# Kernel tuning notes

Hardware: AMD Instinct MI355X
Metric: run time of the kernel (lower is better)

## Reference

```python
import jax, jax.numpy as jnp
import numpy as np

B, T, E, H, D = 2, 2048, 1024, 16, 64   # batch, seq, n_embd, heads, head_dim
C, P, BF, MH, R, F4 = 64, 64, 256, 128, 8, 4096  # ctx_dim, prototypes, basis, mod hidden, gate rank, 4*n_embd


def _rms(x):
    return x * jax.lax.rsqrt(jnp.mean(x * x, axis=-1, keepdims=True) + 1e-6)


def _rotary(x, cos, sin):
    d = x.shape[-1] // 2
    x1, x2 = x[..., :d], x[..., d:]
    return jnp.concatenate([x1 * cos + x2 * sin, -x1 * sin + x2 * cos], axis=-1)


def _ln(x, g, b):
    mu = jnp.mean(x, axis=-1, keepdims=True)
    v = jnp.mean(jnp.square(x - mu), axis=-1, keepdims=True)
    return (x - mu) * jax.lax.rsqrt(v + 1e-5) * g + b


def _remixed(x, ctx, bw, lg, lb, tm, bias, m1w, m1b, m2w, m2b, ogw, ogb, ogB, ogs):
    # RemixedLinear: basis proj -> LayerNorm -> context sigmoid gate -> template mixing -> low-rank output gate
    h = _ln(x @ bw.T, lg, lb)                                              # [B,T,basis]
    gl = jax.nn.gelu(ctx @ m1w.T + m1b, approximate=False) @ m2w.T + m2b   # basis_modulator MLP
    gate_basis = jax.nn.sigmoid(gl)                                        # gate_temperature = 1.0, dense gate
    gate_out = 1.0 + jnp.tanh(ogs * ((ctx @ ogw.T + ogb) @ ogB))           # low-rank output gate
    return (h * gate_basis) @ tm.T * gate_out + bias


def _forward(x, cos, sin, wq, wk, wv, wo, cb_qw, protos,
             fc_bw, fc_lg, fc_lb, fc_tm, fc_b, fc_m1w, fc_m1b, fc_m2w, fc_m2b, fc_ogw, fc_ogb, fc_ogB, fc_ogs,
             pj_bw, pj_lg, pj_lb, pj_tm, pj_b, pj_m1w, pj_m1b, pj_m2w, pj_m2b, pj_ogw, pj_ogb, pj_ogB, pj_ogs):
    b, t, _ = x.shape
    # --- attention with rotary embeddings ---
    xn = _rms(x)
    q = _rotary((xn @ wq.T).reshape(b, t, H, D), cos, sin)
    k = _rotary((xn @ wk.T).reshape(b, t, H, D), cos, sin)
    v = (xn @ wv.T).reshape(b, t, H, D)
    s = jnp.einsum('bqhd,bkhd->bhqk', q, k) * (D ** -0.5)
    mask = jnp.tril(jnp.ones((t, t), dtype=bool))
    s = jnp.where(mask, s, jnp.finfo(s.dtype).min)
    a = jax.nn.softmax(s, axis=-1)
    attn_out = jnp.einsum('bhqk,bkhd->bqhd', a, v).reshape(b, t, E) @ wo.T
    x = x + attn_out
    # --- ContextBank: soft lookup into prototype vocabulary ---
    xn2 = _rms(x)
    cq = xn2 @ cb_qw.T                                  # [B,T,C]
    w = jax.nn.softmax((cq @ protos.T) * (C ** -0.5), axis=-1)
    ctx = w @ protos                                    # [B,T,C]
    # --- RemixedFeedForward: RemixedLinear -> relu^2 -> RemixedLinear ---
    h = _remixed(xn2, ctx, fc_bw, fc_lg, fc_lb, fc_tm, fc_b, fc_m1w, fc_m1b, fc_m2w, fc_m2b, fc_ogw, fc_ogb, fc_ogB, fc_ogs)
    h = jnp.square(jax.nn.relu(h))
    y = _remixed(h, ctx, pj_bw, pj_lg, pj_lb, pj_tm, pj_b, pj_m1w, pj_m1b, pj_m2w, pj_m2b, pj_ogw, pj_ogb, pj_ogB, pj_ogs)
    return x + y


def setup_inputs():
    key = jax.random.key(0)
    ks = jax.random.split(key, 24)
    g = lambda i, shape, s=0.02: jax.random.normal(ks[i], shape, jnp.float32) * s
    t = jnp.arange(T, dtype=jnp.float32)
    inv = 1.0 / (10000.0 ** (jnp.arange(0, D, 2, dtype=jnp.float32) / D))
    ang = t[:, None] * inv                              # [T, D/2]
    return dict(
        x=jax.random.normal(ks[0], (B, T, E), jnp.float32),
        cos=jnp.cos(ang)[None, :, None, :], sin=jnp.sin(ang)[None, :, None, :],
        wq=g(1, (E, E)), wk=g(2, (E, E)), wv=g(3, (E, E)), wo=g(4, (E, E)),
        cb_qw=g(5, (C, E)), protos=g(6, (P, C)),
        fc_bw=g(7, (BF, E)), fc_lg=jnp.ones((BF,)), fc_lb=jnp.zeros((BF,)),
        fc_tm=g(8, (F4, BF), 0.05), fc_b=jnp.zeros((F4,)),
        fc_m1w=g(9, (MH, C)), fc_m1b=jnp.zeros((MH,)),
        fc_m2w=g(10, (BF, MH)), fc_m2b=jnp.zeros((BF,)),
        fc_ogw=g(11, (R, C)), fc_ogb=jnp.zeros((R,)),
        fc_ogB=g(12, (R, F4)), fc_ogs=jnp.full((1,), 0.1, jnp.float32),
        pj_bw=g(13, (BF, F4)), pj_lg=jnp.ones((BF,)), pj_lb=jnp.zeros((BF,)),
        pj_tm=g(14, (E, BF), 0.05), pj_b=jnp.zeros((E,)),
        pj_m1w=g(15, (MH, C)), pj_m1b=jnp.zeros((MH,)),
        pj_m2w=g(16, (BF, MH)), pj_m2b=jnp.zeros((BF,)),
        pj_ogw=g(17, (R, C)), pj_ogb=jnp.zeros((R,)),
        pj_ogB=g(18, (R, E)), pj_ogs=jnp.full((1,), 0.1, jnp.float32),
    )


def reference(x, cos, sin, wq, wk, wv, wo, cb_qw, protos,
              fc_bw, fc_lg, fc_lb, fc_tm, fc_b, fc_m1w, fc_m1b, fc_m2w, fc_m2b, fc_ogw, fc_ogb, fc_ogB, fc_ogs,
              pj_bw, pj_lg, pj_lb, pj_tm, pj_b, pj_m1w, pj_m1b, pj_m2w, pj_m2b, pj_ogw, pj_ogb, pj_ogB, pj_ogs):
    return _forward(x, cos, sin, wq, wk, wv, wo, cb_qw, protos,
                    fc_bw, fc_lg, fc_lb, fc_tm, fc_b, fc_m1w, fc_m1b, fc_m2w, fc_m2b, fc_ogw, fc_ogb, fc_ogB, fc_ogs,
                    pj_bw, pj_lg, pj_lb, pj_tm, pj_b, pj_m1w, pj_m1b, pj_m2w, pj_m2b, pj_ogw, pj_ogb, pj_ogB, pj_ogs)
```

## Files before the change

### kernel.cpp

```cpp
#include <hip/hip_runtime.h>
#include <hip/hip_bf16.h>

typedef unsigned short u16;
typedef unsigned int u32;
typedef __attribute__((ext_vector_type(8))) short bf16x8;
typedef __attribute__((ext_vector_type(4))) float f32x4;
typedef __attribute__((ext_vector_type(4))) u16 u16x4;

#define DEVFN __device__ __forceinline__

DEVFN u16 f2b(float f) {
  u32 u = __builtin_bit_cast(u32, f);
  return (u16)((u + 0x7FFFu + ((u >> 16) & 1u)) >> 16);
}
DEVFN float b2f(u16 b) { return __builtin_bit_cast(float, (u32)b << 16); }
DEVFN u32 cvtpk(float lo, float hi) {
  u32 r;
  asm("v_cvt_pk_bf16_f32 %0, %1, %2" : "=v"(r) : "v"(lo), "v"(hi));
  return r;
}

DEVFN void gll16(const void* g, void* l) {
  __builtin_amdgcn_global_load_lds((const __attribute__((address_space(1))) void*)g,
                                   (__attribute__((address_space(3))) void*)l, 16, 0, 0);
}
#define BARRIER() __builtin_amdgcn_s_barrier()

template <int N> DEVFN void waitvm() {
  if constexpr (N == 0) asm volatile("s_waitcnt vmcnt(0)" ::: "memory");
  else if constexpr (N == 1) asm volatile("s_waitcnt vmcnt(1)" ::: "memory");
  else if constexpr (N == 2) asm volatile("s_waitcnt vmcnt(2)" ::: "memory");
  else if constexpr (N == 3) asm volatile("s_waitcnt vmcnt(3)" ::: "memory");
  else if constexpr (N == 4) asm volatile("s_waitcnt vmcnt(4)" ::: "memory");
  else if constexpr (N == 5) asm volatile("s_waitcnt vmcnt(5)" ::: "memory");
  else if constexpr (N == 6) asm volatile("s_waitcnt vmcnt(6)" ::: "memory");
  else asm volatile("s_waitcnt vmcnt(8)" ::: "memory");
}

constexpr int Tc = 2048, Ec = 1024, Hc = 16, Cc = 64, BFc = 256, F4c = 4096;
constexpr int Mc = 2 * Tc;
constexpr float C8 = 0.18033688f;
constexpr float NEG2LOG2E = -2.8853901f;

constexpr size_t MB = 1ull << 20;
constexpr size_t O_XN  = 0;
constexpr size_t O_HBF = 8 * MB;
constexpr size_t O_QB  = 40 * MB;
constexpr size_t O_H1  = 40 * MB;
constexpr size_t O_A2  = 45 * MB;
constexpr size_t O_KB  = 48 * MB;
constexpr size_t O_H2  = 48 * MB;
constexpr size_t O_VBF = 56 * MB;
constexpr size_t O_CQ  = 64 * MB;
constexpr size_t O_GO1 = 68 * MB + 512 * 1024;
constexpr size_t O_GO2 = 68 * MB + 640 * 1024;
constexpr size_t O_GB1 = 69 * MB;
constexpr size_t O_VT  = 72 * MB;
constexpr size_t O_GB2 = 73 * MB;
constexpr size_t O_A1  = 77 * MB;
constexpr size_t O_X2  = 80 * MB;
constexpr size_t O_WQ  = 96 * MB, O_WK = 98 * MB, O_WV = 100 * MB, O_WO = 102 * MB;
constexpr size_t O_CBQ = 104 * MB;
constexpr size_t O_FCBW = O_CBQ + 128 * 1024;
constexpr size_t O_FCTM = 105 * MB;
constexpr size_t O_PJBW = 107 * MB;
constexpr size_t O_PJTM = 109 * MB;

struct Cvt9 {
  const float* s[9];
  u16* d[9];
  int cum[10];
};
__global__ __launch_bounds__(256) void k_cvt(Cvt9 a) {
  int i = blockIdx.x * 256 + threadIdx.x;
  int seg = 0;
  #pragma unroll
  for (int s = 1; s < 9; s++) seg += (i >= a.cum[s]);
  int off = i - a.cum[seg];
  float4 v = *(const float4*)&a.s[seg][(size_t)off * 4];
  u16x4 o; o.x = f2b(v.x); o.y = f2b(v.y); o.z = f2b(v.z); o.w = f2b(v.w);
  *(u16x4*)&a.d[seg][(size_t)off * 4] = o;
}

DEVFN float bsum256(float v, float* sb) {
  #pragma unroll
  for (int off = 32; off; off >>= 1) v += __shfl_down(v, off);
  __syncthreads();
  if ((threadIdx.x & 63) == 0) sb[threadIdx.x >> 6] = v;
  __syncthreads();
  return (sb[0] + sb[1]) + (sb[2] + sb[3]);
}

__global__ __launch_bounds__(256) void k_rms(const float* __restrict__ x, u16* __restrict__ o) {
  __shared__ float sb[4];
  int row = blockIdx.x, tid = threadIdx.x;
  float4 v = *(const float4*)&x[(size_t)row * 1024 + tid * 4];
  float s = bsum256(v.x * v.x + v.y * v.y + v.z * v.z + v.w * v.w, sb);
  float r = rsqrtf(s * (1.f / 1024.f) + 1e-6f);
  u16x4 ov;
  ov.x = f2b(v.x * r); ov.y = f2b(v.y * r); ov.z = f2b(v.z * r); ov.w = f2b(v.w * r);
  *(u16x4*)&o[(size_t)row * 1024 + tid * 4] = ov;
}

__global__ __launch_bounds__(256) void k_vtrans(const u16* __restrict__ vb, u16* __restrict__ vt) {
  __shared__ u16 tl[64][65];
  int t0 = blockIdx.x * 64, bh = blockIdx.y;
  int b = bh >> 4, h = bh & 15, tid = threadIdx.x;
  #pragma unroll
  for (int rep = 0; rep < 16; rep++) {
    int idx = rep * 256 + tid, r = idx >> 6, c = idx & 63;
    tl[r][c] = vb[((size_t)(b * 2048 + t0 + r)) * 1024 + h * 64 + c];
  }
  __syncthreads();
  #pragma unroll
  for (int rep = 0; rep < 16; rep++) {
    int idx = rep * 256 + tid, d = idx >> 6, tt = idx & 63;
    vt[((size_t)bh * 64 + d) * 2048 + t0 + tt] = tl[tt][d];
  }
}

#define MFMA16(A, B, C) __builtin_amdgcn_mfma_f32_16x16x32_bf16(A, B, C, 0, 0, 0)
__global__ __launch_bounds__(256) void k_attn(const u16* __restrict__ Q, const u16* __restrict__ Kb,
                                              const u16* __restrict__ VT, u16* __restrict__ O) {
  const int i = blockIdx.x;
  const int wrk = (i & 7) * 64 + (i >> 3);
  const int hb = wrk >> 4, xp = wrk & 15;
  const int b = hb >> 4, h = hb & 15;
  const int tid = threadIdx.x, lane = tid & 63, w = tid >> 6;
  const int lr = lane & 15, lg = lane >> 4;
  const size_t TE = 2048ull * 1024ull;
  const u16* Qp = Q + (size_t)b * TE + (size_t)h * 64;
  const u16* Kp = Kb + (size_t)b * TE + (size_t)h * 64;
  const u16* Vp = VT + ((size_t)(b * 16 + h)) * 64ull * 2048ull;
  u16* Op = O + (size_t)b * TE + (size_t)h * 64;
  __shared__ __align__(16) u16 Ks[2][4096];
  __shared__ __align__(16) u16 Vs[2][4096];
  __shared__ __align__(16) u16 Ps[4][1024];
  auto stageKV = [&](int j0, int buf) {
    #pragma unroll
    for (int c = 0; c < 2; c++) {
      int u = c * 256 + tid;
      int row = u >> 3, slot = u & 7;
      int cg = slot ^ (row & 7);
      gll16(&Kp[(size_t)(j0 + row) * 1024 + cg * 8], &Ks[buf][u * 8]);
    }
    #pragma unroll
    for (int c = 0; c < 2; c++) {
      int u = c * 256 + tid;
      int row = u >> 3, slot = u & 7;
      int cg = slot ^ (row & 7);
      gll16(&Vp[(size_t)row * 2048 + j0 + cg * 8], &Vs[buf][u * 8]);
    }
  };
  auto run_tile = [&](int qb) {
    const int q0 = qb * 64, qw0 = q0 + w * 16;
    bf16x8 qf0 = *(const bf16x8*)&Qp[(size_t)(qw0 + lr) * 1024 + lg * 8];
    bf16x8 qf1 = *(const bf16x8*)&Qp[(size_t)(qw0 + lr) * 1024 + 32 + lg * 8];
    f32x4 o0 = {}, o1 = {}, o2 = {}, o3 = {};
    float m = -1e30f, l = 0.f;
    const int NT = qb + 1;
    stageKV(0, 0);
    int cur = 0;
    for (int it = 0; it < NT; it++) {
      if (it + 1 < NT) {
        stageKV((it + 1) * 64, cur ^ 1);
        waitvm<4>();
      } else {
        waitvm<0>();
      }
      BARRIER();
      const int j0 = it * 64;
      const u16* Kl = Ks[cur];
      const u16* Vl = Vs[cur];
      f32x4 c4[4];
      __builtin_amdgcn_s_setprio(1);
      #pragma unroll
      for (int kg = 0; kg < 4; kg++) {
        f32x4 cc = {};
        int r = kg * 16 + lr;
        bf16x8 ka0 = *(const bf16x8*)&Kl[r * 64 + ((lg ^ (lr & 7)) * 8)];
        bf16x8 ka1 = *(const bf16x8*)&Kl[r * 64 + (((4 + lg) ^ (lr & 7)) * 8)];
        cc = MFMA16(ka0, qf0, cc);
        cc = MFMA16(ka1, qf1, cc);
        c4[kg] = cc;
      }
      __builtin_amdgcn_s_setprio(0);
      float xs[16];
      #pragma unroll
      for (int kg = 0; kg < 4; kg++)
        #pragma unroll
        for (int r = 0; r < 4; r++) xs[kg * 4 + r] = c4[kg][r];
      if (it == NT - 1) {
        int q = qw0 + lr;
        #pragma unroll
        for (int kg = 0; kg < 4; kg++)
          #pragma unroll
          for (int r = 0; r < 4; r++)
            if (j0 + kg * 16 + lg * 4 + r > q) xs[kg * 4 + r] = -1e30f;
      }
      float tm = fmaxf(xs[0], xs[1]);
      tm = fmaxf(fmaxf(tm, xs[2]), xs[3]);
      tm = fmaxf(fmaxf(tm, xs[4]), xs[5]);
      tm = fmaxf(fmaxf(tm, xs[6]), xs[7]);
      tm = fmaxf(fmaxf(tm, xs[8]), xs[9]);
      tm = fmaxf(fmaxf(tm, xs[10]), xs[11]);
      tm = fmaxf(fmaxf(tm, xs[12]), xs[13]);
      tm = fmaxf(fmaxf(tm, xs[14]), xs[15]);
      tm = fmaxf(tm, __shfl_xor(tm, 16));
      tm = fmaxf(tm, __shfl_xor(tm, 32));
      if (!__all(tm <= m + 64.f)) {
        float mn = fmaxf(m, tm);
        float al = exp2f((m - mn) * C8);
        m = mn;
        l *= al;
        float ar0 = __shfl(al, lg * 4 + 0), ar1 = __shfl(al, lg * 4 + 1);
        float ar2 = __shfl(al, lg * 4 + 2), ar3 = __shfl(al, lg * 4 + 3);
        o0[0] *= ar0; o0[1] *= ar1; o0[2] *= ar2; o0[3] *= ar3;
        o1[0] *= ar0; o1[1] *= ar1; o1[2] *= ar2; o1[3] *= ar3;
        o2[0] *= ar0; o2[1] *= ar1; o2[2] *= ar2; o2[3] *= ar3;
        o3[0] *= ar0; o3[1] *= ar1; o3[2] *= ar2; o3[3] *= ar3;
      }
      const float mnC = -m * C8;
      float p[16], rs = 0.f;
      #pragma unroll
      for (int r = 0; r < 16; r++) { p[r] = exp2f(fmaf(xs[r], C8, mnC)); rs += p[r]; }
      rs += __shfl_xor(rs, 16);
      rs += __shfl_xor(rs, 32);
      l += rs;
      #pragma unroll
      for (int kg = 0; kg < 4; kg++) {
        int unit = (kg >> 1) * 64 + ((kg & 1) * 2 + (lg >> 1)) * 16 + lr;
        uint2 pk;
        pk.x = cvtpk(p[kg * 4 + 0], p[kg * 4 + 1]);
        pk.y = cvtpk(p[kg * 4 + 2], p[kg * 4 + 3]);
        *(uint2*)&Ps[w][unit * 8 + (lg & 1) * 4] = pk;
      }
      bf16x8 pa0 = *(const bf16x8*)&Ps[w][(lg * 16 + lr) * 8];
      bf16x8 pa1 = *(const bf16x8*)&Ps[w][(64 + lg * 16 + lr) * 8];
      __builtin_amdgcn_s_setprio(1);
      #pragma unroll
      for (int dg = 0; dg < 4; dg++) {
        int dr = dg * 16 + lr;
        bf16x8 v0 = *(const bf16x8*)&Vl[dr * 64 + ((lg ^ (lr & 7)) * 8)];
        bf16x8 v1 = *(const bf16x8*)&Vl[dr * 64 + (((4 + lg) ^ (lr & 7)) * 8)];
        f32x4& od = (dg == 0) ? o0 : (dg == 1) ? o1 : (dg == 2) ? o2 : o3;
        od = MFMA16(pa0, v0, od);
        od = MFMA16(pa1, v1, od);
      }
      __builtin_amdgcn_s_setprio(0);
      BARRIER();
      cur ^= 1;
    }
    float li0 = 1.f / __shfl(l, lg * 4 + 0), li1 = 1.f / __shfl(l, lg * 4 + 1);
    float li2 = 1.f / __shfl(l, lg * 4 + 2), li3 = 1.f / __shfl(l, lg * 4 + 3);
    #pragma unroll
    for (int r = 0; r < 4; r++) {
      float lir = (r == 0) ? li0 : (r == 1) ? li1 : (r == 2) ? li2 : li3;
      size_t ro = (size_t)(qw0 + lg * 4 + r) * 1024;
      Op[ro + lr]      = f2b(o0[r] * lir);
      Op[ro + 16 + lr] = f2b(o1[r] * lir);
      Op[ro + 32 + lr] = f2b(o2[r] * lir);
      Op[ro + 48 + lr] = f2b(o3[r] * lir);
    }
  };
  run_tile(xp);
  run_tile(31 - xp);
}

template <int BM, int BN, int WR, int WC, int EPI>
__global__ __launch_bounds__(256) void gemm_bt(
    const u16* __restrict__ A, const u16* __restrict__ Bw,
    float* __restrict__ Co, u16* __restrict__ Cb, u16* __restrict__ Cb2, u16* __restrict__ Cb3,
    int gM, int N, int K, int KS,
    const float* __restrict__ e0, const float* __restrict__ e1,
    const float* __restrict__ e2, const float* __restrict__ e3,
    const float* __restrict__ e4) {
  constexpr int WM = BM / WR, WN = BN / WC;
  constexpr int FM = WM / 16, FN = WN / 16;
  constexpr int ACH = BM / 64, BCH = BN / 64;
  static_assert(WR * WC == 4 && BM % 64 == 0 && BN % 64 == 0, "cfg");
  __shared__ __align__(16) u16 As[2][BM * 32];
  __shared__ __align__(16) u16 Bs[2][BN * 32];
  const int tid = threadIdx.x;
  const int lane = tid & 63, wid = tid >> 6;
  const int wr = wid / WC, wc = wid % WC;
  const int bm = blockIdx.y * BM, bn = blockIdx.x * BN;
  const int lr = lane & 15, lg = lane >> 4;
  const int arow0 = bm + wr * WM, bcol0 = bn + wc * WN;
  const int kbeg = blockIdx.z * KS, kend = kbeg + KS;
  f32x4 acc[FM][FN] = {};
  auto stage = [&](int k0, int buf) {
    #pragma unroll
    for (int c = 0; c < ACH; c++) {
      int u = c * 256 + tid;
      int row = u >> 2, slot = u & 3;
      int cg = slot ^ (row & 3) ^ ((row >> 2) & 3);
      gll16(&A[(size_t)(bm + row) * K + k0 + cg * 8], &As[buf][u * 8]);
    }
    #pragma unroll
    for (int c = 0; c < BCH; c++) {
      int u = c * 256 + tid;
      int row = u >> 2, slot = u & 3;
      int cg = slot ^ (row & 3) ^ ((row >> 2) & 3);
      gll16(&Bw[(size_t)(bn + row) * K + k0 + cg * 8], &Bs[buf][u * 8]);
    }
  };
  stage(kbeg, 0);
  int cur = 0;
  for (int k0 = kbeg; k0 < kend; k0 += 32) {
    if (k0 + 32 < kend) {
      stage(k0 + 32, cur ^ 1);
      waitvm<ACH + BCH>();
    } else {
      waitvm<0>();
    }
    BARRIER();
    const u16* Ab = As[cur];
    const u16* Bb = Bs[cur];
    bf16x8 af[FM], bfr[FN];
    #pragma unroll
    for (int i = 0; i < FM; i++) {
      int tr = wr * WM + i * 16 + lr;
      af[i] = *(const bf16x8*)&Ab[tr * 32 + ((lg ^ (tr & 3) ^ ((tr >> 2) & 3)) * 8)];
    }
    #pragma unroll
    for (int j = 0; j < FN; j++) {
      int tr = wc * WN + j * 16 + lr;
      bfr[j] = *(const bf16x8*)&Bb[tr * 32 + ((lg ^ (tr & 3) ^ ((tr >> 2) & 3)) * 8)];
    }
    #pragma unroll
    for (int i = 0; i < FM; i++)
      #pragma unroll
      for (int j = 0; j < FN; j++)
        acc[i][j] = __builtin_amdgcn_mfma_f32_16x16x32_bf16(af[i], bfr[j], acc[i][j], 0, 0, 0);
    BARRIER();
    cur ^= 1;
  }
  const int nb0 = bcol0 + lr;
  if constexpr (EPI == 0 || EPI == 2) {
    float* Cz = Co + (size_t)blockIdx.z * ((size_t)gM * N);
    #pragma unroll
    for (int i = 0; i < FM; i++)
      #pragma unroll
      for (int r = 0; r < 4; r++) {
        size_t mrow = (size_t)(arow0 + i * 16 + lg * 4 + r);
        #pragma unroll
        for (int j = 0; j < FN; j++) {
          float v = acc[i][j][r];
          if constexpr (EPI == 2) v += e4[mrow * N + nb0 + j * 16];
          Cz[mrow * N + nb0 + j * 16] = v;
        }
      }
  } else if constexpr (EPI == 9) {
    if (bn == 0) {
      #pragma unroll
      for (int i = 0; i < FM; i++)
        #pragma unroll
        for (int r = 0; r < 4; r++) {
          size_t mrow = (size_t)(arow0 + i * 16 + lg * 4 + r);
          #pragma unroll
          for (int j = 0; j < FN; j++)
            Co[mrow * 64 + nb0 + j * 16] = acc[i][j][r];
        }
    } else {
      float* H = (float*)Cb;
      const int c0 = bcol0 - 64 + lr;
      #pragma unroll
      for (int i = 0; i < FM; i++)
        #pragma unroll
        for (int r = 0; r < 4; r++) {
          size_t mrow = (size_t)(arow0 + i * 16 + lg * 4 + r);
          #pragma unroll
          for (int j = 0; j < FN; j++)
            H[mrow * 256 + c0 + j * 16] = acc[i][j][r];
        }
    }
  } else if constexpr (EPI == 8) {
    if (bn < 2048) {
      u16* dst = (bn < 1024) ? Cb : Cb2;
      const int nq0 = (bcol0 & 1023) + lr;
      #pragma unroll
      for (int i = 0; i < FM; i++)
        #pragma unroll
        for (int r = 0; r < 4; r++) {
          size_t mrow = (size_t)(arow0 + i * 16 + lg * 4 + r);
          int t = (int)(mrow & 2047);
          #pragma unroll
          for (int j = 0; j < 2; j++) {
            int d = lr + j * 16;
            float cth = e0[t * 32 + d], sth = e1[t * 32 + d];
            float x1 = acc[i][j][r], x2 = acc[i][j + 2][r];
            dst[mrow * 1024 + nq0 + j * 16]       = f2b(x1 * cth + x2 * sth);
            dst[mrow * 1024 + nq0 + (j + 2) * 16] = f2b(x2 * cth - x1 * sth);
          }
        }
    } else {
      const int nv0 = (bcol0 - 2048) + lr;
      #pragma unroll
      for (int i = 0; i < FM; i++)
        #pragma unroll
        for (int r = 0; r < 4; r++) {
          size_t mrow = (size_t)(arow0 + i * 16 + lg * 4 + r);
          #pragma unroll
          for (int j = 0; j < FN; j++)
            Cb3[mrow * 1024 + nv0 + j * 16] = f2b(acc[i][j][r]);
        }
    }
  } else {
    const float cg = e3[0] * NEG2LOG2E;
    float gB[FN][8], bias[FN];
    #pragma unroll
    for (int j = 0; j < FN; j++) {
      int n = nb0 + j * 16;
      bias[j] = e2[n];
      #pragma unroll
      for (int rr = 0; rr < 8; rr++) gB[j][rr] = e1[(size_t)rr * N + n];
    }
    #pragma unroll
    for (int i = 0; i < FM; i++)
      #pragma unroll
      for (int r = 0; r < 4; r++) {
        size_t mrow = (size_t)(arow0 + i * 16 + lg * 4 + r);
        float go8[8];
        #pragma unroll
        for (int rr = 0; rr < 8; rr++) go8[rr] = e0[mrow * 8 + rr];
        #pragma unroll
        for (int j = 0; j < FN; j++) {
          float d = 0.f;
          #pragma unroll
          for (int rr = 0; rr < 8; rr++) d += go8[rr] * gB[j][rr];
          float gate = 2.f * __builtin_amdgcn_rcpf(1.f + exp2f(cg * d));
          float v = acc[i][j][r] * gate + bias[j];
          if constexpr (EPI == 3) {
            v = fmaxf(v, 0.f); v *= v;
            Cb[mrow * N + nb0 + j * 16] = f2b(v);
          } else {
            v += e4[mrow * N + nb0 + j * 16];
            Co[mrow * N + nb0 + j * 16] = v;
          }
        }
      }
  }
}

__global__ __launch_bounds__(256) void k_ctxgate(
    const float* __restrict__ cq, const float* __restrict__ pr,
    const float* __restrict__ f_m1w, const float* __restrict__ f_m1b,
    const float* __restrict__ f_m2w, const float* __restrict__ f_m2b,
    const float* __restrict__ f_ogw, const float* __restrict__ f_ogb,
    const float* __restrict__ p_m1w, const float* __restrict__ p_m1b,
    const float* __restrict__ p_m2w, const float* __restrict__ p_m2b,
    const float* __restrict__ p_ogw, const float* __restrict__ p_ogb,
    float* __restrict__ gb1, float* __restrict__ go1,
    float* __restrict__ gb2, float* __restrict__ go2) {
  __shared__ float pl[64 * 65];
  __shared__ __align__(16) float cqs[16][64];
  __shared__ float wl[16][64];
  __shared__ __align__(16) float cs[16][64];
  __shared__ __align__(16) float gls[16][128];
  const int tid = threadIdx.x;
  const int row0 = blockIdx.x * 16;
  for (int idx = tid; idx < 4096; idx += 256) pl[(idx >> 6) * 65 + (idx & 63)] = pr[idx];
  for (int idx = tid; idx < 1024; idx += 256)
    cqs[idx >> 6][idx & 63] = cq[(size_t)row0 * 64 + idx];
  __syncthreads();
  const int row = tid >> 4, pg = tid & 15;
  float sc[4];
  #pragma unroll
  for (int q = 0; q < 4; q++) {
    int p = pg * 4 + q;
    float s = 0.f;
    #pragma unroll
    for (int k4 = 0; k4 < 16; k4++) {
      float4 cv = *(const float4*)&cqs[row][k4 * 4];
      const float* pw = &pl[p * 65 + k4 * 4];
      s += cv.x * pw[0] + cv.y * pw[1] + cv.z * pw[2] + cv.w * pw[3];
    }
    sc[q] = s * 0.125f;
  }
  float mx = fmaxf(fmaxf(sc[0], sc[1]), fmaxf(sc[2], sc[3]));
  #pragma unroll
  for (int off = 1; off <= 8; off <<= 1) mx = fmaxf(mx, __shfl_xor(mx, off));
  float e[4], sum = 0.f;
  #pragma unroll
  for (int q = 0; q < 4; q++) { e[q] = __expf(sc[q] - mx); sum += e[q]; }
  #pragma unroll
  for (int off = 1; off <= 8; off <<= 1) sum += __shfl_xor(sum, off);
  float inv = 1.f / sum;
  #pragma unroll
  for (int q = 0; q < 4; q++) wl[row][pg * 4 + q] = e[q] * inv;
  __syncthreads();
  #pragma unroll
  for (int q = 0; q < 4; q++) {
    int c = pg * 4 + q;
    float a = 0.f;
    for (int p = 0; p < 64; p++) a += wl[row][p] * pl[p * 65 + c];
    cs[row][c] = a;
  }
  __syncthreads();
  auto gate = [&](const float* m1w, const float* m1b, const float* m2w, const float* m2b,
                  const float* ogw, const float* ogb, float* gb, float* go) {
    for (int idx = tid; idx < 2048; idx += 256) {
      int r = idx >> 7, mh = idx & 127;
      const float* wrow = &m1w[(size_t)mh * 64];
      float a = m1b[mh];
      #pragma unroll
      for (int k4 = 0; k4 < 16; k4++) {
        float4 w4 = *(const float4*)&wrow[k4 * 4];
        float4 c4v = *(const float4*)&cs[r][k4 * 4];
        a += c4v.x * w4.x + c4v.y * w4.y + c4v.z * w4.z + c4v.w * w4.w;
      }
      gls[r][mh] = 0.5f * a * (1.f + erff(a * 0.70710678f));
    }
    if (tid < 128) {
      int r = tid >> 3, rr = tid & 7;
      const float* wrow = &ogw[(size_t)rr * 64];
      float a = ogb[rr];
      #pragma unroll
      for (int k4 = 0; k4 < 16; k4++) {
        float4 w4 = *(const float4*)&wrow[k4 * 4];
        float4 c4v = *(const float4*)&cs[r][k4 * 4];
        a += c4v.x * w4.x + c4v.y * w4.y + c4v.z * w4.z + c4v.w * w4.w;
      }
      go[(size_t)(row0 + r) * 8 + rr] = a;
    }
    __syncthreads();
    int n = tid;
    float acc2[16];
    #pragma unroll
    for (int r = 0; r < 16; r++) acc2[r] = m2b[n];
    for (int k4 = 0; k4 < 32; k4++) {
      float4 wv = *(const float4*)&m2w[(size_t)n * 128 + k4 * 4];
      #pragma unroll
      for (int r = 0; r < 16; r++) {
        float4 g = *(const float4*)&gls[r][k4 * 4];
        acc2[r] += g.x * wv.x + g.y * wv.y + g.z * wv.z + g.w * wv.w;
      }
    }
    #pragma unroll
    for (int r = 0; r < 16; r++)
      gb[(size_t)(row0 + r) * 256 + n] = 1.f / (1.f + __expf(-acc2[r]));
    __syncthreads();
  };
  gate(f_m1w, f_m1b, f_m2w, f_m2b, f_ogw, f_ogb, gb1, go1);
  gate(p_m1w, p_m1b, p_m2w, p_m2b, p_ogw, p_ogb, gb2, go2);
}

template <int NS>
__global__ __launch_bounds__(256) void k_lnmul(const float* __restrict__ h,
                                               const float* __restrict__ g,
                                               const float* __restrict__ b,
                                               const float* __restrict__ gbm,
                                               u16* __restrict__ o) {
  __shared__ float sb[4];
  int row = blockIdx.x, n = threadIdx.x;
  float x = 0.f;
  #pragma unroll
  for (int z = 0; z < NS; z++) x += h[(size_t)z * Mc * 256 + (size_t)row * 256 + n];
  float mu = bsum256(x, sb) * (1.f / 256.f);
  float d = x - mu;
  float var = bsum256(d * d, sb) * (1.f / 256.f);
  float y = d * rsqrtf(var + 1e-5f) * g[n] + b[n];
  o[(size_t)row * 256 + n] = f2b(y * gbm[(size_t)row * 256 + n]);
}

extern "C" void kernel_launch(void* const* d_in, const int* in_sizes, int n_in,
                              void* d_out, int out_size, void* d_ws, size_t ws_size,
                              hipStream_t stream) {
  (void)in_sizes; (void)n_in; (void)out_size; (void)ws_size;
  const float* x      = (const float*)d_in[0];
  const float* cosb   = (const float*)d_in[1];
  const float* sinb   = (const float*)d_in[2];
  const float* wq     = (const float*)d_in[3];
  const float* wk     = (const float*)d_in[4];
  const float* wv     = (const float*)d_in[5];
  const float* wo     = (const float*)d_in[6];
  const float* cb_qw  = (const float*)d_in[7];
  const float* protos = (const float*)d_in[8];
  const float* fc_bw  = (const float*)d_in[9];
  const float* fc_lg  = (const float*)d_in[10];
  const float* fc_lb  = (const float*)d_in[11];
  const float* fc_tm  = (const float*)d_in[12];
  const float* fc_b   = (const float*)d_in[13];
  const float* fc_m1w = (const float*)d_in[14];
  const float* fc_m1b = (const float*)d_in[15];
  const float* fc_m2w = (const float*)d_in[16];
  const float* fc_m2b = (const float*)d_in[17];
  const float* fc_ogw = (const float*)d_in[18];
  const float* fc_ogb = (const float*)d_in[19];
  const float* fc_ogB = (const float*)d_in[20];
  const float* fc_ogs = (const float*)d_in[21];
  const float* pj_bw  = (const float*)d_in[22];
  const float* pj_lg  = (const float*)d_in[23];
  const float* pj_lb  = (const float*)d_in[24];
  const float* pj_tm  = (const float*)d_in[25];
  const float* pj_b   = (const float*)d_in[26];
  const float* pj_m1w = (const float*)d_in[27];
  const float* pj_m1b = (const float*)d_in[28];
  const float* pj_m2w = (const float*)d_in[29];
  const float* pj_m2b = (const float*)d_in[30];
  const float* pj_ogw = (const float*)d_in[31];
  const float* pj_ogb = (const float*)d_in[32];
  const float* pj_ogB = (const float*)d_in[33];
  const float* pj_ogs = (const float*)d_in[34];
  char* ws = (char*)d_ws;
  float* outp = (float*)d_out;
  auto U = [&](size_t o) { return (u16*)(ws + o); };
  auto F = [&](size_t o) { return (float*)(ws + o); };
  const float* nf = nullptr;
  u16* nu = nullptr;

  {
    Cvt9 a;
    const float* srcs[9] = {wq, wk, wv, wo, cb_qw, fc_bw, fc_tm, pj_bw, pj_tm};
    size_t offs[9] = {O_WQ, O_WK, O_WV, O_WO, O_CBQ, O_FCBW, O_FCTM, O_PJBW, O_PJTM};
    int ns[9] = {Ec*Ec, Ec*Ec, Ec*Ec, Ec*Ec, Cc*Ec, BFc*Ec, F4c*BFc, BFc*F4c, Ec*BFc};
    int cum = 0;
    for (int s = 0; s < 9; s++) {
      a.s[s] = srcs[s]; a.d[s] = U(offs[s]); a.cum[s] = cum; cum += ns[s] / 4;
    }
    a.cum[9] = cum;
    k_cvt<<<dim3(cum / 256), dim3(256), 0, stream>>>(a);
  }
  k_rms<<<dim3(Mc), dim3(256), 0, stream>>>(x, U(O_XN));
  gemm_bt<128,128,2,2,8><<<dim3(24,32), dim3(256), 0, stream>>>(U(O_XN), U(O_WQ), nullptr, U(O_QB), U(O_KB), U(O_VBF), Mc, 3072, Ec, Ec, cosb, sinb, nf, nf, nf);
  k_vtrans<<<dim3(Tc / 64, 2 * Hc), dim3(256), 0, stream>>>(U(O_VBF), U(O_VT));
  k_attn<<<dim3(512), dim3(256), 0, stream>>>(U(O_QB), U(O_KB), U(O_VT), U(O_XN));
  gemm_bt<128,128,2,2,2><<<dim3(8,32), dim3(256), 0, stream>>>(U(O_XN), U(O_WO), F(O_X2), nu, nu, nu, Mc, Ec, Ec, Ec, nf, nf, nf, nf, x);
  k_rms<<<dim3(Mc), dim3(256), 0, stream>>>(F(O_X2), U(O_XN));
  gemm_bt<64,64,1,4,9><<<dim3(5,64), dim3(256), 0, stream>>>(U(O_XN), U(O_CBQ), F(O_CQ), (u16*)F(O_H1), nu, nu, Mc, 320, Ec, Ec, nf, nf, nf, nf, nf);
  k_ctxgate<<<dim3(Mc / 16), dim3(256), 0, stream>>>(F(O_CQ), protos,
      fc_m1w, fc_m1b, fc_m2w, fc_m2b, fc_ogw, fc_ogb,
      pj_m1w, pj_m1b, pj_m2w, pj_m2b, pj_ogw, pj_ogb,
      F(O_GB1), F(O_GO1), F(O_GB2), F(O_GO2));
  k_lnmul<1><<<dim3(Mc), dim3(256), 0, stream>>>(F(O_H1), fc_lg, fc_lb, F(O_GB1), U(O_A1));
  gemm_bt<128,128,2,2,3><<<dim3(32,32), dim3(256), 0, stream>>>(U(O_A1), U(O_FCTM), nullptr, U(O_HBF), nu, nu, Mc, F4c, BFc, BFc, F(O_GO1), fc_ogB, fc_b, fc_ogs, nf);
  gemm_bt<64,64,1,4,0><<<dim3(4,64,4), dim3(256), 0, stream>>>(U(O_HBF), U(O_PJBW), F(O_H2), nu, nu, nu, Mc, BFc, F4c, 1024, nf, nf, nf, nf, nf);
  k_lnmul<4><<<dim3(Mc), dim3(256), 0, stream>>>(F(O_H2), pj_lg, pj_lb, F(O_GB2), U(O_A2));
  gemm_bt<128,128,2,2,4><<<dim3(8,32), dim3(256), 0, stream>>>(U(O_A2), U(O_PJTM), outp, nu, nu, nu, Mc, Ec, BFc, BFc, F(O_GO2), pj_ogB, pj_b, pj_ogs, F(O_X2));
}
```

Baseline: 419.0 us.

## Fuse V transpose into QKV epilogue, split-K out-proj, fuse LN into ctxgate

The QKV GEMM epilogue now writes V directly in transposed layout, which removes the separate transpose kernel. Attention launches one q-tile per block (1024 blocks) instead of pairing two tiles per block. The output projection runs split-K into two partial buffers, and a new kernel sums them with the residual and applies RMSNorm. The first LayerNorm-times-gate step is folded into the context-gate kernel, which drops one launch and the gb1 round trip. The trade-offs are extra partial-sum traffic and uncoalesced strided 8-byte V stores.

```diff
diff --git a/kernel.cpp b/kernel.cpp
--- a/kernel.cpp
+++ b/kernel.cpp
@@ -46,15 +46,14 @@
 constexpr size_t O_XN  = 0;
 constexpr size_t O_HBF = 8 * MB;
 constexpr size_t O_QB  = 40 * MB;
+constexpr size_t O_WOP = 40 * MB;
 constexpr size_t O_H1  = 40 * MB;
 constexpr size_t O_A2  = 45 * MB;
 constexpr size_t O_KB  = 48 * MB;
 constexpr size_t O_H2  = 48 * MB;
-constexpr size_t O_VBF = 56 * MB;
 constexpr size_t O_CQ  = 64 * MB;
 constexpr size_t O_GO1 = 68 * MB + 512 * 1024;
 constexpr size_t O_GO2 = 68 * MB + 640 * 1024;
-constexpr size_t O_GB1 = 69 * MB;
 constexpr size_t O_VT  = 72 * MB;
 constexpr size_t O_GB2 = 73 * MB;
 constexpr size_t O_A1  = 77 * MB;
@@ -102,30 +101,35 @@
   *(u16x4*)&o[(size_t)row * 1024 + tid * 4] = ov;
 }
 
-__global__ __launch_bounds__(256) void k_vtrans(const u16* __restrict__ vb, u16* __restrict__ vt) {
-  __shared__ u16 tl[64][65];
-  int t0 = blockIdx.x * 64, bh = blockIdx.y;
-  int b = bh >> 4, h = bh & 15, tid = threadIdx.x;
-  #pragma unroll
-  for (int rep = 0; rep < 16; rep++) {
-    int idx = rep * 256 + tid, r = idx >> 6, c = idx & 63;
-    tl[r][c] = vb[((size_t)(b * 2048 + t0 + r)) * 1024 + h * 64 + c];
-  }
-  __syncthreads();
-  #pragma unroll
-  for (int rep = 0; rep < 16; rep++) {
-    int idx = rep * 256 + tid, d = idx >> 6, tt = idx & 63;
-    vt[((size_t)bh * 64 + d) * 2048 + t0 + tt] = tl[tt][d];
-  }
+__global__ __launch_bounds__(256) void k_rms2c(const float* __restrict__ p,
+                                               const float* __restrict__ x,
+                                               float* __restrict__ x2,
+                                               u16* __restrict__ xn) {
+  __shared__ float sb[4];
+  int row = blockIdx.x, tid = threadIdx.x;
+  size_t base = (size_t)row * 1024 + tid * 4;
+  float4 a = *(const float4*)&p[base];
+  float4 c = *(const float4*)&p[(size_t)Mc * 1024 + base];
+  float4 xv = *(const float4*)&x[base];
+  float4 v;
+  v.x = a.x + c.x + xv.x; v.y = a.y + c.y + xv.y;
+  v.z = a.z + c.z + xv.z; v.w = a.w + c.w + xv.w;
+  *(float4*)&x2[base] = v;
+  float s = bsum256(v.x * v.x + v.y * v.y + v.z * v.z + v.w * v.w, sb);
+  float r = rsqrtf(s * (1.f / 1024.f) + 1e-6f);
+  u16x4 ov;
+  ov.x = f2b(v.x * r); ov.y = f2b(v.y * r); ov.z = f2b(v.z * r); ov.w = f2b(v.w * r);
+  *(u16x4*)&xn[base] = ov;
 }
 
 #define MFMA16(A, B, C) __builtin_amdgcn_mfma_f32_16x16x32_bf16(A, B, C, 0, 0, 0)
 __global__ __launch_bounds__(256) void k_attn(const u16* __restrict__ Q, const u16* __restrict__ Kb,
                                               const u16* __restrict__ VT, u16* __restrict__ O) {
   const int i = blockIdx.x;
-  const int wrk = (i & 7) * 64 + (i >> 3);
-  const int hb = wrk >> 4, xp = wrk & 15;
-  const int b = hb >> 4, h = hb & 15;
+  const int wrk = (i & 7) * 128 + (i >> 3);
+  const int bh = wrk >> 5, j = wrk & 31;
+  const int qb = (j & 1) ? (j >> 1) : (31 - (j >> 1));
+  const int b = bh >> 4, h = bh & 15;
   const int tid = threadIdx.x, lane = tid & 63, w = tid >> 6;
   const int lr = lane & 15, lg = lane >> 4;
   const size_t TE = 2048ull * 1024ull;
@@ -152,119 +156,115 @@
       gll16(&Vp[(size_t)row * 2048 + j0 + cg * 8], &Vs[buf][u * 8]);
     }
   };
-  auto run_tile = [&](int qb) {
-    const int q0 = qb * 64, qw0 = q0 + w * 16;
-    bf16x8 qf0 = *(const bf16x8*)&Qp[(size_t)(qw0 + lr) * 1024 + lg * 8];
-    bf16x8 qf1 = *(const bf16x8*)&Qp[(size_t)(qw0 + lr) * 1024 + 32 + lg * 8];
-    f32x4 o0 = {}, o1 = {}, o2 = {}, o3 = {};
-    float m = -1e30f, l = 0.f;
-    const int NT = qb + 1;
-    stageKV(0, 0);
-    int cur = 0;
-    for (int it = 0; it < NT; it++) {
-      if (it + 1 < NT) {
-        stageKV((it + 1) * 64, cur ^ 1);
-        waitvm<4>();
-      } else {
-        waitvm<0>();
-      }
-      BARRIER();
-      const int j0 = it * 64;
-      const u16* Kl = Ks[cur];
-      const u16* Vl = Vs[cur];
-      f32x4 c4[4];
-      __builtin_amdgcn_s_setprio(1);
-      #pragma unroll
-      for (int kg = 0; kg < 4; kg++) {
-        f32x4 cc = {};
-        int r = kg * 16 + lr;
-        bf16x8 ka0 = *(const bf16x8*)&Kl[r * 64 + ((lg ^ (lr & 7)) * 8)];
-        bf16x8 ka1 = *(const bf16x8*)&Kl[r * 64 + (((4 + lg) ^ (lr & 7)) * 8)];
-        cc = MFMA16(ka0, qf0, cc);
-        cc = MFMA16(ka1, qf1, cc);
-        c4[kg] = cc;
-      }
-      __builtin_amdgcn_s_setprio(0);
-      float xs[16];
+  const int q0 = qb * 64, qw0 = q0 + w * 16;
+  bf16x8 qf0 = *(const bf16x8*)&Qp[(size_t)(qw0 + lr) * 1024 + lg * 8];
+  bf16x8 qf1 = *(const bf16x8*)&Qp[(size_t)(qw0 + lr) * 1024 + 32 + lg * 8];
+  f32x4 o0 = {}, o1 = {}, o2 = {}, o3 = {};
+  float m = -1e30f, l = 0.f;
+  const int NT = qb + 1;
+  stageKV(0, 0);
+  int cur = 0;
+  for (int it = 0; it < NT; it++) {
+    if (it + 1 < NT) {
+      stageKV((it + 1) * 64, cur ^ 1);
+      waitvm<4>();
+    } else {
+      waitvm<0>();
+    }
+    BARRIER();
+    const int j0 = it * 64;
+    const u16* Kl = Ks[cur];
+    const u16* Vl = Vs[cur];
+    f32x4 c4[4];
+    __builtin_amdgcn_s_setprio(1);
+    #pragma unroll
+    for (int kg = 0; kg < 4; kg++) {
+      f32x4 cc = {};
+      int r = kg * 16 + lr;
+      bf16x8 ka0 = *(const bf16x8*)&Kl[r * 64 + ((lg ^ (lr & 7)) * 8)];
+      bf16x8 ka1 = *(const bf16x8*)&Kl[r * 64 + (((4 + lg) ^ (lr & 7)) * 8)];
+      cc = MFMA16(ka0, qf0, cc);
+      cc = MFMA16(ka1, qf1, cc);
+      c4[kg] = cc;
+    }
+    __builtin_amdgcn_s_setprio(0);
+    float xs[16];
+    #pragma unroll
+    for (int kg = 0; kg < 4; kg++)
+      #pragma unroll
+      for (int r = 0; r < 4; r++) xs[kg * 4 + r] = c4[kg][r];
+    if (it == NT - 1) {
+      int q = qw0 + lr;
       #pragma unroll
       for (int kg = 0; kg < 4; kg++)
         #pragma unroll
-        for (int r = 0; r < 4; r++) xs[kg * 4 + r] = c4[kg][r];
-      if (it == NT - 1) {
-        int q = qw0 + lr;
-        #pragma unroll
-        for (int kg = 0; kg < 4; kg++)
-          #pragma unroll
-          for (int r = 0; r < 4; r++)
-            if (j0 + kg * 16 + lg * 4 + r > q) xs[kg * 4 + r] = -1e30f;
-      }
-      float tm = fmaxf(xs[0], xs[1]);
-      tm = fmaxf(fmaxf(tm, xs[2]), xs[3]);
-      tm = fmaxf(fmaxf(tm, xs[4]), xs[5]);
-      tm = fmaxf(fmaxf(tm, xs[6]), xs[7]);
-      tm = fmaxf(fmaxf(tm, xs[8]), xs[9]);
-      tm = fmaxf(fmaxf(tm, xs[10]), xs[11]);
-      tm = fmaxf(fmaxf(tm, xs[12]), xs[13]);
-      tm = fmaxf(fmaxf(tm, xs[14]), xs[15]);
-      tm = fmaxf(tm, __shfl_xor(tm, 16));
-      tm = fmaxf(tm, __shfl_xor(tm, 32));
-      if (!__all(tm <= m + 64.f)) {
-        float mn = fmaxf(m, tm);
-        float al = exp2f((m - mn) * C8);
-        m = mn;
-        l *= al;
-        float ar0 = __shfl(al, lg * 4 + 0), ar1 = __shfl(al, lg * 4 + 1);
-        float ar2 = __shfl(al, lg * 4 + 2), ar3 = __shfl(al, lg * 4 + 3);
-        o0[0] *= ar0; o0[1] *= ar1; o0[2] *= ar2; o0[3] *= ar3;
-        o1[0] *= ar0; o1[1] *= ar1; o1[2] *= ar2; o1[3] *= ar3;
-        o2[0] *= ar0; o2[1] *= ar1; o2[2] *= ar2; o2[3] *= ar3;
-        o3[0] *= ar0; o3[1] *= ar1; o3[2] *= ar2; o3[3] *= ar3;
-      }
-      const float mnC = -m * C8;
-      float p[16], rs = 0.f;
-      #pragma unroll
-      for (int r = 0; r < 16; r++) { p[r] = exp2f(fmaf(xs[r], C8, mnC)); rs += p[r]; }
-      rs += __shfl_xor(rs, 16);
-      rs += __shfl_xor(rs, 32);
-      l += rs;
-      #pragma unroll
-      for (int kg = 0; kg < 4; kg++) {
-        int unit = (kg >> 1) * 64 + ((kg & 1) * 2 + (lg >> 1)) * 16 + lr;
-        uint2 pk;
-        pk.x = cvtpk(p[kg * 4 + 0], p[kg * 4 + 1]);
-        pk.y = cvtpk(p[kg * 4 + 2], p[kg * 4 + 3]);
-        *(uint2*)&Ps[w][unit * 8 + (lg & 1) * 4] = pk;
-      }
-      bf16x8 pa0 = *(const bf16x8*)&Ps[w][(lg * 16 + lr) * 8];
-      bf16x8 pa1 = *(const bf16x8*)&Ps[w][(64 + lg * 16 + lr) * 8];
-      __builtin_amdgcn_s_setprio(1);
-      #pragma unroll
-      for (int dg = 0; dg < 4; dg++) {
-        int dr = dg * 16 + lr;
-        bf16x8 v0 = *(const bf16x8*)&Vl[dr * 64 + ((lg ^ (lr & 7)) * 8)];
-        bf16x8 v1 = *(const bf16x8*)&Vl[dr * 64 + (((4 + lg) ^ (lr & 7)) * 8)];
-        f32x4& od = (dg == 0) ? o0 : (dg == 1) ? o1 : (dg == 2) ? o2 : o3;
-        od = MFMA16(pa0, v0, od);
-        od = MFMA16(pa1, v1, od);
-      }
-      __builtin_amdgcn_s_setprio(0);
-      BARRIER();
-      cur ^= 1;
-    }
-    float li0 = 1.f / __shfl(l, lg * 4 + 0), li1 = 1.f / __shfl(l, lg * 4 + 1);
-    float li2 = 1.f / __shfl(l, lg * 4 + 2), li3 = 1.f / __shfl(l, lg * 4 + 3);
-    #pragma unroll
-    for (int r = 0; r < 4; r++) {
-      float lir = (r == 0) ? li0 : (r == 1) ? li1 : (r == 2) ? li2 : li3;
-      size_t ro = (size_t)(qw0 + lg * 4 + r) * 1024;
-      Op[ro + lr]      = f2b(o0[r] * lir);
-      Op[ro + 16 + lr] = f2b(o1[r] * lir);
-      Op[ro + 32 + lr] = f2b(o2[r] * lir);
-      Op[ro + 48 + lr] = f2b(o3[r] * lir);
-    }
-  };
-  run_tile(xp);
-  run_tile(31 - xp);
+        for (int r = 0; r < 4; r++)
+          if (j0 + kg * 16 + lg * 4 + r > q) xs[kg * 4 + r] = -1e30f;
+    }
+    float tm = fmaxf(xs[0], xs[1]);
+    tm = fmaxf(fmaxf(tm, xs[2]), xs[3]);
+    tm = fmaxf(fmaxf(tm, xs[4]), xs[5]);
+    tm = fmaxf(fmaxf(tm, xs[6]), xs[7]);
+    tm = fmaxf(fmaxf(tm, xs[8]), xs[9]);
+    tm = fmaxf(fmaxf(tm, xs[10]), xs[11]);
+    tm = fmaxf(fmaxf(tm, xs[12]), xs[13]);
+    tm = fmaxf(fmaxf(tm, xs[14]), xs[15]);
+    tm = fmaxf(tm, __shfl_xor(tm, 16));
+    tm = fmaxf(tm, __shfl_xor(tm, 32));
+    if (!__all(tm <= m + 64.f)) {
+      float mn = fmaxf(m, tm);
+      float al = exp2f((m - mn) * C8);
+      m = mn;
+      l *= al;
+      float ar0 = __shfl(al, lg * 4 + 0), ar1 = __shfl(al, lg * 4 + 1);
+      float ar2 = __shfl(al, lg * 4 + 2), ar3 = __shfl(al, lg * 4 + 3);
+      o0[0] *= ar0; o0[1] *= ar1; o0[2] *= ar2; o0[3] *= ar3;
+      o1[0] *= ar0; o1[1] *= ar1; o1[2] *= ar2; o1[3] *= ar3;
+      o2[0] *= ar0; o2[1] *= ar1; o2[2] *= ar2; o2[3] *= ar3;
+      o3[0] *= ar0; o3[1] *= ar1; o3[2] *= ar2; o3[3] *= ar3;
+    }
+    const float mnC = -m * C8;
+    float p[16], rs = 0.f;
+    #pragma unroll
+    for (int r = 0; r < 16; r++) { p[r] = exp2f(fmaf(xs[r], C8, mnC)); rs += p[r]; }
+    rs += __shfl_xor(rs, 16);
+    rs += __shfl_xor(rs, 32);
+    l += rs;
+    #pragma unroll
+    for (int kg = 0; kg < 4; kg++) {
+      int unit = (kg >> 1) * 64 + ((kg & 1) * 2 + (lg >> 1)) * 16 + lr;
+      uint2 pk;
+      pk.x = cvtpk(p[kg * 4 + 0], p[kg * 4 + 1]);
+      pk.y = cvtpk(p[kg * 4 + 2], p[kg * 4 + 3]);
+      *(uint2*)&Ps[w][unit * 8 + (lg & 1) * 4] = pk;
+    }
+    bf16x8 pa0 = *(const bf16x8*)&Ps[w][(lg * 16 + lr) * 8];
+    bf16x8 pa1 = *(const bf16x8*)&Ps[w][(64 + lg * 16 + lr) * 8];
+    __builtin_amdgcn_s_setprio(1);
+    #pragma unroll
+    for (int dg = 0; dg < 4; dg++) {
+      int dr = dg * 16 + lr;
+      bf16x8 v0 = *(const bf16x8*)&Vl[dr * 64 + ((lg ^ (lr & 7)) * 8)];
+      bf16x8 v1 = *(const bf16x8*)&Vl[dr * 64 + (((4 + lg) ^ (lr & 7)) * 8)];
+      f32x4& od = (dg == 0) ? o0 : (dg == 1) ? o1 : (dg == 2) ? o2 : o3;
+      od = MFMA16(pa0, v0, od);
+      od = MFMA16(pa1, v1, od);
+    }
+    __builtin_amdgcn_s_setprio(0);
+    BARRIER();
+    cur ^= 1;
+  }
+  float li0 = 1.f / __shfl(l, lg * 4 + 0), li1 = 1.f / __shfl(l, lg * 4 + 1);
+  float li2 = 1.f / __shfl(l, lg * 4 + 2), li3 = 1.f / __shfl(l, lg * 4 + 3);
+  #pragma unroll
+  for (int r = 0; r < 4; r++) {
+    float lir = (r == 0) ? li0 : (r == 1) ? li1 : (r == 2) ? li2 : li3;
+    size_t ro = (size_t)(qw0 + lg * 4 + r) * 1024;
+    Op[ro + lr]      = f2b(o0[r] * lir);
+    Op[ro + 16 + lr] = f2b(o1[r] * lir);
+    Op[ro + 32 + lr] = f2b(o2[r] * lir);
+    Op[ro + 48 + lr] = f2b(o3[r] * lir);
+  }
 }
 
 template <int BM, int BN, int WR, int WC, int EPI>
@@ -337,7 +337,7 @@
     cur ^= 1;
   }
   const int nb0 = bcol0 + lr;
-  if constexpr (EPI == 0 || EPI == 2) {
+  if constexpr (EPI == 0) {
     float* Cz = Co + (size_t)blockIdx.z * ((size_t)gM * N);
     #pragma unroll
     for (int i = 0; i < FM; i++)
@@ -345,11 +345,8 @@
       for (int r = 0; r < 4; r++) {
         size_t mrow = (size_t)(arow0 + i * 16 + lg * 4 + r);
         #pragma unroll
-        for (int j = 0; j < FN; j++) {
-          float v = acc[i][j][r];
-          if constexpr (EPI == 2) v += e4[mrow * N + nb0 + j * 16];
-          Cz[mrow * N + nb0 + j * 16] = v;
-        }
+        for (int j = 0; j < FN; j++)
+          Cz[mrow * N + nb0 + j * 16] = acc[i][j][r];
       }
   } else if constexpr (EPI == 9) {
     if (bn == 0) {
@@ -395,15 +392,18 @@
           }
         }
     } else {
-      const int nv0 = (bcol0 - 2048) + lr;
+      const int hh = (bcol0 - 2048) >> 6;
+      const int bb = arow0 >> 11;
+      const int t0 = (arow0 & 2047) + lg * 4;
+      u16* vt = Cb3 + ((size_t)(bb * 16 + hh) * 64) * 2048;
       #pragma unroll
       for (int i = 0; i < FM; i++)
         #pragma unroll
-        for (int r = 0; r < 4; r++) {
-          size_t mrow = (size_t)(arow0 + i * 16 + lg * 4 + r);
-          #pragma unroll
-          for (int j = 0; j < FN; j++)
-            Cb3[mrow * 1024 + nv0 + j * 16] = f2b(acc[i][j][r]);
+        for (int j = 0; j < FN; j++) {
+          u16x4 pk;
+          pk.x = f2b(acc[i][j][0]); pk.y = f2b(acc[i][j][1]);
+          pk.z = f2b(acc[i][j][2]); pk.w = f2b(acc[i][j][3]);
+          *(u16x4*)&vt[(size_t)(lr + j * 16) * 2048 + t0 + i * 16] = pk;
         }
     }
   } else {
@@ -445,19 +445,22 @@
 
 __global__ __launch_bounds__(256) void k_ctxgate(
     const float* __restrict__ cq, const float* __restrict__ pr,
+    const float* __restrict__ h1, const float* __restrict__ lg1,
+    const float* __restrict__ lb1,
     const float* __restrict__ f_m1w, const float* __restrict__ f_m1b,
     const float* __restrict__ f_m2w, const float* __restrict__ f_m2b,
     const float* __restrict__ f_ogw, const float* __restrict__ f_ogb,
     const float* __restrict__ p_m1w, const float* __restrict__ p_m1b,
     const float* __restrict__ p_m2w, const float* __restrict__ p_m2b,
     const float* __restrict__ p_ogw, const float* __restrict__ p_ogb,
-    float* __restrict__ gb1, float* __restrict__ go1,
+    u16* __restrict__ a1, float* __restrict__ go1,
     float* __restrict__ gb2, float* __restrict__ go2) {
   __shared__ float pl[64 * 65];
   __shared__ __align__(16) float cqs[16][64];
   __shared__ float wl[16][64];
   __shared__ __align__(16) float cs[16][64];
   __shared__ __align__(16) float gls[16][128];
+  __shared__ float sLN[16][2];
   const int tid = threadIdx.x;
   const int row0 = blockIdx.x * 16;
   for (int idx = tid; idx < 4096; idx += 256) pl[(idx >> 6) * 65 + (idx & 63)] = pr[idx];
@@ -498,52 +501,116 @@
     cs[row][c] = a;
   }
   __syncthreads();
-  auto gate = [&](const float* m1w, const float* m1b, const float* m2w, const float* m2b,
-                  const float* ogw, const float* ogb, float* gb, float* go) {
-    for (int idx = tid; idx < 2048; idx += 256) {
-      int r = idx >> 7, mh = idx & 127;
-      const float* wrow = &m1w[(size_t)mh * 64];
-      float a = m1b[mh];
-      #pragma unroll
-      for (int k4 = 0; k4 < 16; k4++) {
-        float4 w4 = *(const float4*)&wrow[k4 * 4];
-        float4 c4v = *(const float4*)&cs[r][k4 * 4];
-        a += c4v.x * w4.x + c4v.y * w4.y + c4v.z * w4.z + c4v.w * w4.w;
-      }
-      gls[r][mh] = 0.5f * a * (1.f + erff(a * 0.70710678f));
-    }
-    if (tid < 128) {
-      int r = tid >> 3, rr = tid & 7;
-      const float* wrow = &ogw[(size_t)rr * 64];
-      float a = ogb[rr];
-      #pragma unroll
-      for (int k4 = 0; k4 < 16; k4++) {
-        float4 w4 = *(const float4*)&wrow[k4 * 4];
-        float4 c4v = *(const float4*)&cs[r][k4 * 4];
-        a += c4v.x * w4.x + c4v.y * w4.y + c4v.z * w4.z + c4v.w * w4.w;
-      }
-      go[(size_t)(row0 + r) * 8 + rr] = a;
-    }
-    __syncthreads();
+  float* hs = pl;
+  for (int idx = tid; idx < 4096; idx += 256)
+    hs[idx] = h1[(size_t)row0 * 256 + idx];
+  __syncthreads();
+  {
+    int r = tid >> 4, sub = tid & 15;
+    float s = 0.f, s2 = 0.f;
+    #pragma unroll
+    for (int k = 0; k < 16; k++) {
+      float v = hs[r * 256 + sub * 16 + k];
+      s += v; s2 += v * v;
+    }
+    #pragma unroll
+    for (int mk = 1; mk <= 8; mk <<= 1) { s += __shfl_xor(s, mk); s2 += __shfl_xor(s2, mk); }
+    if (sub == 0) {
+      float mu = s * (1.f / 256.f);
+      sLN[r][0] = mu;
+      sLN[r][1] = rsqrtf(fmaxf(s2 * (1.f / 256.f) - mu * mu, 0.f) + 1e-5f);
+    }
+  }
+  __syncthreads();
+  for (int idx = tid; idx < 2048; idx += 256) {
+    int r = idx >> 7, mh = idx & 127;
+    const float* wrow = &f_m1w[(size_t)mh * 64];
+    float a = f_m1b[mh];
+    #pragma unroll
+    for (int k4 = 0; k4 < 16; k4++) {
+      float4 w4 = *(const float4*)&wrow[k4 * 4];
+      float4 c4v = *(const float4*)&cs[r][k4 * 4];
+      a += c4v.x * w4.x + c4v.y * w4.y + c4v.z * w4.z + c4v.w * w4.w;
+    }
+    gls[r][mh] = 0.5f * a * (1.f + erff(a * 0.70710678f));
+  }
+  if (tid < 128) {
+    int r = tid >> 3, rr = tid & 7;
+    const float* wrow = &f_ogw[(size_t)rr * 64];
+    float a = f_ogb[rr];
+    #pragma unroll
+    for (int k4 = 0; k4 < 16; k4++) {
+      float4 w4 = *(const float4*)&wrow[k4 * 4];
+      float4 c4v = *(const float4*)&cs[r][k4 * 4];
+      a += c4v.x * w4.x + c4v.y * w4.y + c4v.z * w4.z + c4v.w * w4.w;
+    }
+    go1[(size_t)(row0 + r) * 8 + rr] = a;
+  }
+  __syncthreads();
+  {
     int n = tid;
     float acc2[16];
     #pragma unroll
-    for (int r = 0; r < 16; r++) acc2[r] = m2b[n];
+    for (int r = 0; r < 16; r++) acc2[r] = f_m2b[n];
     for (int k4 = 0; k4 < 32; k4++) {
-      float4 wv = *(const float4*)&m2w[(size_t)n * 128 + k4 * 4];
+      float4 wv = *(const float4*)&f_m2w[(size_t)n * 128 + k4 * 4];
       #pragma unroll
       for (int r = 0; r < 16; r++) {
         float4 g = *(const float4*)&gls[r][k4 * 4];
         acc2[r] += g.x * wv.x + g.y * wv.y + g.z * wv.z + g.w * wv.w;
       }
     }
+    float gvn = lg1[n], bvn = lb1[n];
+    #pragma unroll
+    for (int r = 0; r < 16; r++) {
+      float sig = 1.f / (1.f + __expf(-acc2[r]));
+      float y = (hs[r * 256 + n] - sLN[r][0]) * sLN[r][1] * gvn + bvn;
+      a1[(size_t)(row0 + r) * 256 + n] = f2b(y * sig);
+    }
+  }
+  __syncthreads();
+  for (int idx = tid; idx < 2048; idx += 256) {
+    int r = idx >> 7, mh = idx & 127;
+    const float* wrow = &p_m1w[(size_t)mh * 64];
+    float a = p_m1b[mh];
+    #pragma unroll
+    for (int k4 = 0; k4 < 16; k4++) {
+      float4 w4 = *(const float4*)&wrow[k4 * 4];
+      float4 c4v = *(const float4*)&cs[r][k4 * 4];
+      a += c4v.x * w4.x + c4v.y * w4.y + c4v.z * w4.z + c4v.w * w4.w;
+    }
+    gls[r][mh] = 0.5f * a * (1.f + erff(a * 0.70710678f));
+  }
+  if (tid < 128) {
+    int r = tid >> 3, rr = tid & 7;
+    const float* wrow = &p_ogw[(size_t)rr * 64];
+    float a = p_ogb[rr];
+    #pragma unroll
+    for (int k4 = 0; k4 < 16; k4++) {
+      float4 w4 = *(const float4*)&wrow[k4 * 4];
+      float4 c4v = *(const float4*)&cs[r][k4 * 4];
+      a += c4v.x * w4.x + c4v.y * w4.y + c4v.z * w4.z + c4v.w * w4.w;
+    }
+    go2[(size_t)(row0 + r) * 8 + rr] = a;
+  }
+  __syncthreads();
+  {
+    int n = tid;
+    float acc2[16];
+    #pragma unroll
+    for (int r = 0; r < 16; r++) acc2[r] = p_m2b[n];
+    for (int k4 = 0; k4 < 32; k4++) {
+      float4 wv = *(const float4*)&p_m2w[(size_t)n * 128 + k4 * 4];
+      #pragma unroll
+      for (int r = 0; r < 16; r++) {
+        float4 g = *(const float4*)&gls[r][k4 * 4];
+        acc2[r] += g.x * wv.x + g.y * wv.y + g.z * wv.z + g.w * wv.w;
+      }
+    }
     #pragma unroll
     for (int r = 0; r < 16; r++)
-      gb[(size_t)(row0 + r) * 256 + n] = 1.f / (1.f + __expf(-acc2[r]));
-    __syncthreads();
-  };
-  gate(f_m1w, f_m1b, f_m2w, f_m2b, f_ogw, f_ogb, gb1, go1);
-  gate(p_m1w, p_m1b, p_m2w, p_m2b, p_ogw, p_ogb, gb2, go2);
+      gb2[(size_t)(row0 + r) * 256 + n] = 1.f / (1.f + __expf(-acc2[r]));
+  }
 }
 
 template <int NS>
@@ -623,17 +690,16 @@
     k_cvt<<<dim3(cum / 256), dim3(256), 0, stream>>>(a);
   }
   k_rms<<<dim3(Mc), dim3(256), 0, stream>>>(x, U(O_XN));
-  gemm_bt<128,128,2,2,8><<<dim3(24,32), dim3(256), 0, stream>>>(U(O_XN), U(O_WQ), nullptr, U(O_QB), U(O_KB), U(O_VBF), Mc, 3072, Ec, Ec, cosb, sinb, nf, nf, nf);
-  k_vtrans<<<dim3(Tc / 64, 2 * Hc), dim3(256), 0, stream>>>(U(O_VBF), U(O_VT));
-  k_attn<<<dim3(512), dim3(256), 0, stream>>>(U(O_QB), U(O_KB), U(O_VT), U(O_XN));
-  gemm_bt<128,128,2,2,2><<<dim3(8,32), dim3(256), 0, stream>>>(U(O_XN), U(O_WO), F(O_X2), nu, nu, nu, Mc, Ec, Ec, Ec, nf, nf, nf, nf, x);
-  k_rms<<<dim3(Mc), dim3(256), 0, stream>>>(F(O_X2), U(O_XN));
+  gemm_bt<128,128,2,2,8><<<dim3(24,32), dim3(256), 0, stream>>>(U(O_XN), U(O_WQ), nullptr, U(O_QB), U(O_KB), U(O_VT), Mc, 3072, Ec, Ec, cosb, sinb, nf, nf, nf);
+  k_attn<<<dim3(1024), dim3(256), 0, stream>>>(U(O_QB), U(O_KB), U(O_VT), U(O_XN));
+  gemm_bt<128,128,2,2,0><<<dim3(8,32,2), dim3(256), 0, stream>>>(U(O_XN), U(O_WO), F(O_WOP), nu, nu, nu, Mc, Ec, Ec, 512, nf, nf, nf, nf, nf);
+  k_rms2c<<<dim3(Mc), dim3(256), 0, stream>>>(F(O_WOP), x, F(O_X2), U(O_XN));
   gemm_bt<64,64,1,4,9><<<dim3(5,64), dim3(256), 0, stream>>>(U(O_XN), U(O_CBQ), F(O_CQ), (u16*)F(O_H1), nu, nu, Mc, 320, Ec, Ec, nf, nf, nf, nf, nf);
   k_ctxgate<<<dim3(Mc / 16), dim3(256), 0, stream>>>(F(O_CQ), protos,
+      F(O_H1), fc_lg, fc_lb,
       fc_m1w, fc_m1b, fc_m2w, fc_m2b, fc_ogw, fc_ogb,
       pj_m1w, pj_m1b, pj_m2w, pj_m2b, pj_ogw, pj_ogb,
-      F(O_GB1), F(O_GO1), F(O_GB2), F(O_GO2));
-  k_lnmul<1><<<dim3(Mc), dim3(256), 0, stream>>>(F(O_H1), fc_lg, fc_lb, F(O_GB1), U(O_A1));
+      U(O_A1), F(O_GO1), F(O_GB2), F(O_GO2));
   gemm_bt<128,128,2,2,3><<<dim3(32,32), dim3(256), 0, stream>>>(U(O_A1), U(O_FCTM), nullptr, U(O_HBF), nu, nu, Mc, F4c, BFc, BFc, F(O_GO1), fc_ogB, fc_b, fc_ogs, nf);
   gemm_bt<64,64,1,4,0><<<dim3(4,64,4), dim3(256), 0, stream>>>(U(O_HBF), U(O_PJBW), F(O_H2), nu, nu, nu, Mc, BFc, F4c, 1024, nf, nf, nf, nf, nf);
   k_lnmul<4><<<dim3(Mc), dim3(256), 0, stream>>>(F(O_H2), pj_lg, pj_lb, F(O_GB2), U(O_A2));
```

Measured after the change: 424.5 us. No clear change (+1.3%).
